# Optimization experiments

Measured on AMD Instinct MI355X. Metric: run time of the kernel, lower is better.

Reference implementation:

```python
import jax, jax.numpy as jnp
import numpy as np

D_MODEL = 256
HEADS = 4
HEAD_DIM = D_MODEL // HEADS  # 64
BN_EPS = 1e-5


def conv1(x, W, b):
    # Conv1d kernel_size=1 == per-position linear: x [B,C,N], W [O,C], b [O]
    return jnp.einsum('oc,bcn->bon', W, x) + b[:, None]


def setup_inputs() -> dict:
    key = jax.random.key(0)
    ks = jax.random.split(key, 12)
    B, N, M = 4, 4096, 4096
    s = 0.02
    return {
        'x': jax.random.normal(ks[0], (B, D_MODEL, N), jnp.float32),
        'source': jax.random.normal(ks[1], (B, D_MODEL, M), jnp.float32),
        'pq_w': jax.random.normal(ks[2], (D_MODEL, D_MODEL), jnp.float32) * s,
        'pq_b': jnp.zeros((D_MODEL,), jnp.float32),
        'pk_w': jax.random.normal(ks[3], (D_MODEL, D_MODEL), jnp.float32) * s,
        'pk_b': jnp.zeros((D_MODEL,), jnp.float32),
        'pv_w': jax.random.normal(ks[4], (D_MODEL, D_MODEL), jnp.float32) * s,
        'pv_b': jnp.zeros((D_MODEL,), jnp.float32),
        'merge_w': jax.random.normal(ks[5], (D_MODEL, D_MODEL), jnp.float32) * s,
        'merge_b': jnp.zeros((D_MODEL,), jnp.float32),
        'mlp1_w': jax.random.normal(ks[6], (2 * D_MODEL, 2 * D_MODEL), jnp.float32) * s,
        'mlp1_b': jax.random.normal(ks[7], (2 * D_MODEL,), jnp.float32) * s,
        'bn_gamma': jnp.ones((2 * D_MODEL,), jnp.float32),
        'bn_beta': jnp.zeros((2 * D_MODEL,), jnp.float32),
        'mlp2_w': jax.random.normal(ks[8], (D_MODEL, 2 * D_MODEL), jnp.float32) * s,
        'mlp2_b': jnp.zeros((D_MODEL,), jnp.float32),  # nn.init.constant_(mlp[-1].bias, 0.0)
    }


def reference(x, source, pq_w, pq_b, pk_w, pk_b, pv_w, pv_b,
              merge_w, merge_b, mlp1_w, mlp1_b, bn_gamma, bn_beta,
              mlp2_w, mlp2_b):
    B = x.shape[0]
    # projections; torch view(B, dim, heads, -1): channels split as (head_dim, heads)
    q = conv1(x, pq_w, pq_b).reshape(B, HEAD_DIM, HEADS, -1)       # [B,d,h,N]
    k = conv1(source, pk_w, pk_b).reshape(B, HEAD_DIM, HEADS, -1)  # [B,d,h,M]
    v = conv1(source, pv_w, pv_b).reshape(B, HEAD_DIM, HEADS, -1)
    scores = jnp.einsum('bdhn,bdhm->bhnm', q, k) / (HEAD_DIM ** 0.5)
    prob = jax.nn.softmax(scores, axis=-1)                          # [B,h,N,M]
    attn_out = jnp.einsum('bhnm,bdhm->bdhn', prob, v).reshape(B, D_MODEL, -1)
    message = conv1(attn_out, merge_w, merge_b)                     # [B,D,N]
    # MLP: conv(512->512) + BatchNorm1d (training-mode batch stats) + ReLU + conv(512->256)
    h = conv1(jnp.concatenate([x, message], axis=1), mlp1_w, mlp1_b)  # [B,2D,N]
    mean = jnp.mean(h, axis=(0, 2), keepdims=True)
    var = jnp.var(h, axis=(0, 2), keepdims=True)  # biased, as torch BN uses for normalization
    h = bn_gamma[:, None] * (h - mean) * jax.lax.rsqrt(var + BN_EPS) + bn_beta[:, None]
    h = jax.nn.relu(h)
    return conv1(h, mlp2_w, mlp2_b)
```

## Files before the change

### kernel.cpp

```cpp
#include <hip/hip_runtime.h>
#include <hip/hip_bf16.h>

#define D_MODEL 256
#define HEADS 4
#define HD 64
#define BATCH 4
#define SEQ 4096
#define NPOS (BATCH*SEQ)
#define SCALE_LOG2 0.18033688011112042f
#define MCHUNKS 2

typedef __attribute__((ext_vector_type(4))) float floatx4;
typedef __attribute__((ext_vector_type(8))) short bf16x8;
typedef __attribute__((ext_vector_type(4))) short bf16x4;
typedef __attribute__((ext_vector_type(4))) unsigned short ushortx4;

__device__ __forceinline__ float bf2f(unsigned short b) {
    return __uint_as_float(((unsigned int)b) << 16);
}
__device__ __forceinline__ unsigned short f2bf(float f) {
    unsigned int u = __float_as_uint(f);
    return (unsigned short)((u + 0x7fffu + ((u >> 16) & 1u)) >> 16);
}
__device__ __forceinline__ bf16x4 pack_bf16x4(float a, float b, float c, float d) {
    __hip_bfloat162 lo = __float22bfloat162_rn(float2{a, b});
    __hip_bfloat162 hi = __float22bfloat162_rn(float2{c, d});
    union { __hip_bfloat162 h2[2]; bf16x4 v; } u;
    u.h2[0] = lo; u.h2[1] = hi;
    return u.v;
}
__device__ __forceinline__ bf16x8 pack_bf16x8(floatx4 a, floatx4 b) {
    union { bf16x4 h[2]; bf16x8 v; } u;
    u.h[0] = pack_bf16x4(a[0], a[1], a[2], a[3]);
    u.h[1] = pack_bf16x4(b[0], b[1], b[2], b[3]);
    return u.v;
}
#define MFMA(a,b,c) __builtin_amdgcn_mfma_f32_16x16x32_bf16((a),(b),(c),0,0,0)
#define EXP2(x) __builtin_amdgcn_exp2f(x)

__global__ __launch_bounds__(256) void prep(
        const float* __restrict__ pq_w, const float* __restrict__ pk_w,
        const float* __restrict__ pv_w, const float* __restrict__ merge_w,
        const float* __restrict__ mlp1_w, const float* __restrict__ mlp2_w,
        const float* __restrict__ x, const float* __restrict__ src,
        unsigned short* __restrict__ wqb, unsigned short* __restrict__ wkb,
        unsigned short* __restrict__ wvb, unsigned short* __restrict__ wmt,
        unsigned short* __restrict__ w1b, unsigned short* __restrict__ w2b,
        unsigned short* __restrict__ xT, unsigned short* __restrict__ srcT)
{
    __shared__ unsigned short lT[64][264];
    const int t = threadIdx.x;
    const int bx = blockIdx.x;
    if (bx < 576) {
        int linear = bx * 1024 + t * 4;
        const float* srcW; unsigned short* dst; int off;
        if (linear < 65536)       { srcW = pq_w;   dst = wqb; off = 0; }
        else if (linear < 131072) { srcW = pk_w;   dst = wkb; off = 65536; }
        else if (linear < 196608) { srcW = pv_w;   dst = wvb; off = 131072; }
        else if (linear < 458752) { srcW = mlp1_w; dst = w1b; off = 196608; }
        else                      { srcW = mlp2_w; dst = w2b; off = 458752; }
        int i = linear - off;
        float4 w = *(const float4*)&srcW[i];
        ushortx4 s = { f2bf(w.x), f2bf(w.y), f2bf(w.z), f2bf(w.w) };
        *(ushortx4*)&dst[i] = s;
        return;
    }
    if (bx < 640) {
        int i = (bx - 576) * 1024 + t * 4;
        int cp = i >> 8, o = i & 255;
        int pc = ((cp & 63) << 2) | (cp >> 6);
        unsigned short s[4];
#pragma unroll
        for (int j = 0; j < 4; ++j)
            s[j] = f2bf(merge_w[(size_t)(o + j) * 256 + pc]);
        *(ushortx4*)&wmt[i] = *(const ushortx4*)s;
        return;
    }
    int z = bx - 640;
    const float* X = (z < 256) ? x : src;
    unsigned short* O = (z < 256) ? xT : srcT;
    int rem = z & 255;
    int b = rem >> 6, n0 = (rem & 63) * 64;
#pragma unroll
    for (int r = 0; r < 16; ++r) {
        int idx = r * 256 + t;
        int ch = idx >> 4, nnq = (idx & 15) * 4;
        float4 v4 = *(const float4*)&X[((size_t)b * 256 + ch) * SEQ + n0 + nnq];
        lT[nnq + 0][ch] = f2bf(v4.x);
        lT[nnq + 1][ch] = f2bf(v4.y);
        lT[nnq + 2][ch] = f2bf(v4.z);
        lT[nnq + 3][ch] = f2bf(v4.w);
    }
    __syncthreads();
#pragma unroll
    for (int r = 0; r < 8; ++r) {
        int idx = r * 256 + t;
        int row = idx >> 5, cg = (idx & 31) * 8;
        *(bf16x8*)&O[((size_t)b * SEQ + n0 + row) * 256 + cg] = *(const bf16x8*)&lT[row][cg];
    }
}

__global__ __launch_bounds__(256) void prep2(
        const float* __restrict__ mlp1_w, const float* __restrict__ mlp1_b,
        const float* __restrict__ merge_b, const unsigned short* __restrict__ wmt,
        unsigned short* __restrict__ w1f, float* __restrict__ b1f)
{
    __shared__ unsigned short lA[64][40];
    __shared__ unsigned short lB[128][40];
    const int t = threadIdx.x;
    if (blockIdx.y == 8) {
        int o2 = blockIdx.x * 256 + t;
        float s = mlp1_b[o2];
        for (int o = 0; o < 256; ++o)
            s += mlp1_w[(size_t)o2 * 512 + 256 + o] * merge_b[o];
        b1f[o2] = s;
        return;
    }
    const int lane = t & 63, wid = t >> 6;
    const int wm = wid >> 1, wn = wid & 1;
    const int lrow = lane & 15, quad = lane >> 4;
    const int o20 = blockIdx.y * 64;
    const int c0  = blockIdx.x * 128;

    floatx4 acc[2][4];
#pragma unroll
    for (int i = 0; i < 2; ++i)
#pragma unroll
        for (int j = 0; j < 4; ++j) acc[i][j] = (floatx4){0.f,0.f,0.f,0.f};

    for (int k0 = 0; k0 < 256; k0 += 32) {
#pragma unroll
        for (int r = 0; r < 2; ++r) {
            int linear = r * 1024 + t * 4;
            int row = linear >> 5, col = linear & 31;
            float4 w = *(const float4*)&mlp1_w[(size_t)(o20 + row) * 512 + 256 + k0 + col];
            ushortx4 s = { f2bf(w.x), f2bf(w.y), f2bf(w.z), f2bf(w.w) };
            *(ushortx4*)&lA[row][col] = s;
        }
#pragma unroll
        for (int r = 0; r < 2; ++r) {
            int linear = r * 256 + t;
            int row = linear >> 2, cg = (linear & 3) * 8;
            *(bf16x8*)&lB[row][cg] = *(const bf16x8*)&wmt[(size_t)(c0 + row) * 256 + k0 + cg];
        }
        __syncthreads();
        bf16x8 aF[2], bF[4];
        const int kq = quad * 8;
#pragma unroll
        for (int mt = 0; mt < 2; ++mt)
            aF[mt] = *(const bf16x8*)&lA[wm*32 + mt*16 + lrow][kq];
#pragma unroll
        for (int nt = 0; nt < 4; ++nt)
            bF[nt] = *(const bf16x8*)&lB[wn*64 + nt*16 + lrow][kq];
#pragma unroll
        for (int mt = 0; mt < 2; ++mt)
#pragma unroll
            for (int nt = 0; nt < 4; ++nt)
                acc[mt][nt] = MFMA(aF[mt], bF[nt], acc[mt][nt]);
        __syncthreads();
    }
#pragma unroll
    for (int nt = 0; nt < 4; ++nt) {
        int cp = c0 + wn*64 + nt*16 + lrow;
#pragma unroll
        for (int mt = 0; mt < 2; ++mt)
#pragma unroll
            for (int j = 0; j < 4; ++j) {
                int o2 = o20 + wm*32 + mt*16 + quad*4 + j;
                w1f[(size_t)o2 * 256 + cp] = f2bf(acc[mt][nt][j]);
            }
    }
}

__global__ __launch_bounds__(256) void proj_qkv_all(
        const unsigned short* __restrict__ Wq, const float* __restrict__ bq,
        const unsigned short* __restrict__ Wk, const float* __restrict__ bk,
        const unsigned short* __restrict__ Wv, const float* __restrict__ bv,
        const unsigned short* __restrict__ xT, const unsigned short* __restrict__ srcT,
        unsigned short* __restrict__ qo, unsigned short* __restrict__ ko,
        unsigned short* __restrict__ vo)
{
    __shared__ unsigned short smem[128 * 80];
    unsigned short (*lA)[40] = (unsigned short (*)[40])smem;
    unsigned short (*lB)[40] = (unsigned short (*)[40])(smem + 128 * 40);
    unsigned short (*stage)[72] = (unsigned short (*)[72])smem;
    const int t = threadIdx.x;
    const int lane = t & 63, wid = t >> 6;
    const int wm = wid >> 1, wn = wid & 1;
    const int lrow = lane & 15, quad = lane >> 4;
    const int mode = blockIdx.x >> 1;
    const int ob = (blockIdx.x & 1) * 128;
    const int n0 = blockIdx.y * 128;
    const int b  = blockIdx.z;
    const unsigned short* W  = (mode == 0) ? Wq : (mode == 1) ? Wk : Wv;
    const float* bias        = (mode == 0) ? bq : (mode == 1) ? bk : bv;
    const unsigned short* XT = (mode == 0) ? xT : srcT;
    unsigned short* out      = (mode == 0) ? qo : (mode == 1) ? ko : vo;

    const int srow[2] = { (0*256 + t) >> 2, (1*256 + t) >> 2 };
    const int scg = (t & 3) * 8;

    floatx4 acc[4][4];
#pragma unroll
    for (int i = 0; i < 4; ++i)
#pragma unroll
        for (int j = 0; j < 4; ++j) acc[i][j] = (floatx4){0.f,0.f,0.f,0.f};

    bf16x8 rW[2], rX[2];
#pragma unroll
    for (int r = 0; r < 2; ++r) {
        rW[r] = *(const bf16x8*)&W[(size_t)(ob + srow[r]) * 256 + scg];
        rX[r] = *(const bf16x8*)&XT[((size_t)b * SEQ + n0 + srow[r]) * 256 + scg];
    }
#pragma unroll
    for (int r = 0; r < 2; ++r) {
        *(bf16x8*)&lA[srow[r]][scg] = rW[r];
        *(bf16x8*)&lB[srow[r]][scg] = rX[r];
    }
    __syncthreads();

    for (int kc = 0; kc < 8; ++kc) {
        const bool pre = (kc + 1 < 8);
        if (pre) {
            const int k1 = (kc + 1) * 32;
#pragma unroll
            for (int r = 0; r < 2; ++r) {
                rW[r] = *(const bf16x8*)&W[(size_t)(ob + srow[r]) * 256 + k1 + scg];
                rX[r] = *(const bf16x8*)&XT[((size_t)b * SEQ + n0 + srow[r]) * 256 + k1 + scg];
            }
        }
        bf16x8 aF[4], bF[4];
        const int kq = quad * 8;
#pragma unroll
        for (int mt = 0; mt < 4; ++mt)
            aF[mt] = *(const bf16x8*)&lA[wm*64 + mt*16 + lrow][kq];
#pragma unroll
        for (int nt = 0; nt < 4; ++nt)
            bF[nt] = *(const bf16x8*)&lB[wn*64 + nt*16 + lrow][kq];
#pragma unroll
        for (int mt = 0; mt < 4; ++mt)
#pragma unroll
            for (int nt = 0; nt < 4; ++nt)
                acc[mt][nt] = MFMA(aF[mt], bF[nt], acc[mt][nt]);
        __syncthreads();
        if (pre) {
#pragma unroll
            for (int r = 0; r < 2; ++r) {
                *(bf16x8*)&lA[srow[r]][scg] = rW[r];
                *(bf16x8*)&lB[srow[r]][scg] = rX[r];
            }
            __syncthreads();
        }
    }
    const float osc = (mode == 0) ? SCALE_LOG2 : 1.0f;
    if (mode == 2) {
#pragma unroll
        for (int mt = 0; mt < 4; ++mt) {
#pragma unroll
            for (int j = 0; j < 4; ++j) {
                int o = ob + wm*64 + mt*16 + quad*4 + j;
                float bvv = bias[o];
                int d = o >> 2, h = o & 3;
#pragma unroll
                for (int nt = 0; nt < 4; ++nt) {
                    int n = n0 + wn*64 + nt*16 + lrow;
                    out[((size_t)(b*HEADS + h) * HD + d) * SEQ + n] = f2bf(acc[mt][nt][j] + bvv);
                }
            }
        }
        return;
    }
    for (int half = 0; half < 2; ++half) {
        __syncthreads();
        if (wm == half) {
#pragma unroll
            for (int mt = 0; mt < 4; ++mt)
#pragma unroll
                for (int j = 0; j < 4; ++j) {
                    int o = ob + half*64 + mt*16 + quad*4 + j;
                    float bvv = bias[o];
                    int col = j*16 + mt*4 + quad;
#pragma unroll
                    for (int nt = 0; nt < 4; ++nt) {
                        int n = wn*64 + nt*16 + lrow;
                        stage[n][col] = f2bf((acc[mt][nt][j] + bvv) * osc);
                    }
                }
        }
        __syncthreads();
#pragma unroll
        for (int i = 0; i < 4; ++i) {
            int c = i * 256 + t;
            int n = c >> 3, h = (c >> 1) & 3, sub = c & 1;
            bf16x8 val = *(const bf16x8*)&stage[n][h*16 + sub*8];
            int d0 = (ob >> 2) + half*16 + sub*8;
            *(bf16x8*)&out[((size_t)(b*HEADS + h) * SEQ + n0 + n) * HD + d0] = val;
        }
    }
}

__global__ __launch_bounds__(256, 4) void flash_attn(
        const unsigned short* __restrict__ q,
        const unsigned short* __restrict__ k,
        const unsigned short* __restrict__ v,
        unsigned short* __restrict__ poO, float* __restrict__ pol)
{
    __shared__ unsigned short smem[2][9216];
    const int t = threadIdx.x, lane = t & 63, wid = t >> 6;
    const int lrow = lane & 15, quad = lane >> 4;
    const int bc = blockIdx.x, qt = blockIdx.y;
    const int bh = bc & 15, chunk = bc >> 4;
    const int hb = (bh & 3) * BATCH + (bh >> 2);
    const int r0 = qt * 128 + wid * 32;

    bf16x8 qf[2][2];
#pragma unroll
    for (int nh = 0; nh < 2; ++nh) {
        const size_t base = ((size_t)bh * SEQ + r0 + nh*16 + lrow) * HD;
        qf[nh][0] = *(const bf16x8*)&q[base + quad * 8];
        qf[nh][1] = *(const bf16x8*)&q[base + 32 + quad * 8];
    }
    bf16x8 ones;
#pragma unroll
    for (int i = 0; i < 8; ++i) ones[i] = (short)0x3F80;
    int mmv[2], cgv[2], krv[2];
#pragma unroll
    for (int r = 0; r < 2; ++r) {
        int linear = r * 256 + t;
        int mm = linear >> 3, cg = (linear & 7) * 8;
        int c2 = mm >> 5, mp = mm & 31;
        mmv[r] = mm; cgv[r] = cg;
        krv[r] = (c2 << 5) + ((mp & 4) << 2) + ((mp >> 3) << 2) + (mp & 3);
    }
    const size_t kbase = ((size_t)bh * SEQ + chunk * (SEQ/MCHUNKS));
    const size_t vbase = (size_t)bh * HD;
    const int moff = chunk * (SEQ/MCHUNKS);
    const int NIT = SEQ / MCHUNKS / 64;

    floatx4 oacc[2][4], oaccL[2];
#pragma unroll
    for (int nh = 0; nh < 2; ++nh) {
        oaccL[nh] = (floatx4){0.f,0.f,0.f,0.f};
#pragma unroll
        for (int i = 0; i < 4; ++i) oacc[nh][i] = (floatx4){0.f,0.f,0.f,0.f};
    }

    {
        bf16x8 pk[2], pv[2];
#pragma unroll
        for (int r = 0; r < 2; ++r) {
            pk[r] = *(const bf16x8*)&k[(kbase + mmv[r]) * HD + cgv[r]];
            pv[r] = *(const bf16x8*)&v[(vbase + mmv[r]) * SEQ + moff + cgv[r]];
        }
#pragma unroll
        for (int r = 0; r < 2; ++r) {
            *(bf16x8*)&smem[0][krv[r]*72 + cgv[r]]        = pk[r];
            *(bf16x8*)&smem[0][4608 + mmv[r]*72 + cgv[r]] = pv[r];
        }
    }
    __syncthreads();

    int p = 0;
#pragma unroll 1
    for (int it = 0; it < NIT; ++it) {
        bf16x8 pk[2], pv[2];
        const bool pre = (it + 1 < NIT);
        if (pre) {
            const int m1 = (it + 1) * 64;
#pragma unroll
            for (int r = 0; r < 2; ++r) {
                pk[r] = *(const bf16x8*)&k[(kbase + m1 + mmv[r]) * HD + cgv[r]];
                pv[r] = *(const bf16x8*)&v[(vbase + mmv[r]) * SEQ + moff + m1 + cgv[r]];
            }
        }
        const unsigned short* lK = smem[p];
        const unsigned short* lV = smem[p] + 4608;

        bf16x8 pf8[2][2];
#pragma unroll
        for (int c2 = 0; c2 < 2; ++c2) {
            floatx4 sa[2][2];
#pragma unroll
            for (int AB = 0; AB < 2; ++AB) {
                sa[AB][0] = (floatx4){0.f,0.f,0.f,0.f};
                sa[AB][1] = (floatx4){0.f,0.f,0.f,0.f};
#pragma unroll
                for (int kc = 0; kc < 2; ++kc) {
                    bf16x8 kf = *(const bf16x8*)&lK[(c2*32 + AB*16 + lrow)*72 + kc*32 + quad*8];
                    sa[AB][0] = MFMA(kf, qf[0][kc], sa[AB][0]);
                    sa[AB][1] = MFMA(kf, qf[1][kc], sa[AB][1]);
                }
            }
#pragma unroll
            for (int nh = 0; nh < 2; ++nh) {
                floatx4 ea, eb;
#pragma unroll
                for (int i = 0; i < 4; ++i) { ea[i] = EXP2(sa[0][nh][i]); eb[i] = EXP2(sa[1][nh][i]); }
                pf8[c2][nh] = pack_bf16x8(ea, eb);
            }
        }
#pragma unroll
        for (int c2 = 0; c2 < 2; ++c2) {
            oaccL[0] = MFMA(ones, pf8[c2][0], oaccL[0]);
            oaccL[1] = MFMA(ones, pf8[c2][1], oaccL[1]);
#pragma unroll
            for (int dt = 0; dt < 4; ++dt) {
                bf16x8 vf = *(const bf16x8*)&lV[(dt*16 + lrow)*72 + c2*32 + quad*8];
                oacc[0][dt] = MFMA(vf, pf8[c2][0], oacc[0][dt]);
                oacc[1][dt] = MFMA(vf, pf8[c2][1], oacc[1][dt]);
            }
        }
        if (pre) {
#pragma unroll
            for (int r = 0; r < 2; ++r) {
                *(bf16x8*)&smem[p^1][krv[r]*72 + cgv[r]]        = pk[r];
                *(bf16x8*)&smem[p^1][4608 + mmv[r]*72 + cgv[r]] = pv[r];
            }
        }
        __syncthreads();
        p ^= 1;
    }
    const size_t prow = (size_t)(chunk*16 + hb) * SEQ + qt * 128;
    if (lane < 16) {
        pol[prow + wid*32 + lrow]      = oaccL[0][0];
        pol[prow + wid*32 + 16 + lrow] = oaccL[1][0];
    }
    unsigned short* stB = (unsigned short*)&smem[0][0];
#pragma unroll
    for (int nh = 0; nh < 2; ++nh)
#pragma unroll
        for (int dt = 0; dt < 4; ++dt) {
            bf16x4 pv4 = pack_bf16x4(oacc[nh][dt][0], oacc[nh][dt][1],
                                     oacc[nh][dt][2], oacc[nh][dt][3]);
            *(bf16x4*)&stB[(wid*32 + nh*16 + lrow)*72 + dt*16 + quad*4] = pv4;
        }
    __syncthreads();
#pragma unroll
    for (int i = 0; i < 4; ++i) {
        int c = i * 256 + t;
        int row = c >> 3, sub = c & 7;
        *(bf16x8*)&poO[(prow + row) * HD + sub*8] = *(const bf16x8*)&stB[row*72 + sub*8];
    }
}

__global__ __launch_bounds__(256) void gemm_mlp1(
        const unsigned short* __restrict__ xT, const unsigned short* __restrict__ poO,
        const float* __restrict__ pol,
        const unsigned short* __restrict__ w1b, const unsigned short* __restrict__ w1f,
        const float* __restrict__ b1f, unsigned short* __restrict__ h1,
        float* __restrict__ sums, float* __restrict__ sumsq)
{
    __shared__ unsigned short lA[2][64][40];
    __shared__ unsigned short lB[2][128][40];
    __shared__ float sInv[256];
    const int t = threadIdx.x;
    const int lane = t & 63, wid = t >> 6;
    const int wm = wid >> 1, wn = wid & 1;
    const int lrow = lane & 15, quad = lane >> 4;
    const int o0 = blockIdx.x * 128;
    const int p0 = blockIdx.y * 64;
    const int b = p0 >> 12, n0 = p0 & (SEQ - 1);
    const size_t CH = (size_t)16 * SEQ * HD;

    {
        int h = t >> 6, nn = t & 63;
        int hb = h * BATCH + b;
        float l0 = pol[(size_t)hb * SEQ + n0 + nn];
        float l1 = pol[(size_t)(16 + hb) * SEQ + n0 + nn];
        sInv[t] = 1.0f / (l0 + l1);
    }
    __syncthreads();

    const int arow = t >> 2, acg = (t & 3) * 8;
    const int brow[2] = { (0*256 + t) >> 2, (1*256 + t) >> 2 };

    floatx4 acc[2][4];
#pragma unroll
    for (int i = 0; i < 2; ++i)
#pragma unroll
        for (int j = 0; j < 4; ++j) acc[i][j] = (floatx4){0.f,0.f,0.f,0.f};

    bf16x8 rA, rB[2];
    auto load_tile = [&](int k0) {
        if (k0 < 256) {
            rA = *(const bf16x8*)&xT[(size_t)(p0 + arow) * 256 + k0 + acg];
#pragma unroll
            for (int r = 0; r < 2; ++r)
                rB[r] = *(const bf16x8*)&w1b[(size_t)(o0 + brow[r]) * 512 + k0 + acg];
        } else {
            const int kk2 = k0 - 256;
            const int h = kk2 >> 6, d0 = kk2 & 63, hb = h * BATCH + b;
            const unsigned short* bse = &poO[((size_t)hb * SEQ + n0 + arow) * HD + d0 + acg];
            bf16x8 a0 = *(const bf16x8*)bse;
            bf16x8 a1 = *(const bf16x8*)(bse + CH);
            float inv = sInv[h*64 + arow];
            unsigned short res[8];
#pragma unroll
            for (int i = 0; i < 8; ++i)
                res[i] = f2bf((bf2f((unsigned short)a0[i]) + bf2f((unsigned short)a1[i])) * inv);
            rA = *(const bf16x8*)res;
#pragma unroll
            for (int r = 0; r < 2; ++r)
                rB[r] = *(const bf16x8*)&w1f[(size_t)(o0 + brow[r]) * 256 + kk2 + acg];
        }
    };

    load_tile(0);
    *(bf16x8*)&lA[0][arow][acg] = rA;
#pragma unroll
    for (int r = 0; r < 2; ++r) *(bf16x8*)&lB[0][brow[r]][acg] = rB[r];
    __syncthreads();

    int p = 0;
    for (int kc = 0; kc < 16; ++kc) {
        const bool pre = (kc + 1 < 16);
        if (pre) load_tile((kc + 1) * 32);
        bf16x8 aF[2], bF[4];
        const int kq = quad * 8;
#pragma unroll
        for (int mt = 0; mt < 2; ++mt)
            aF[mt] = *(const bf16x8*)&lA[p][wm*32 + mt*16 + lrow][kq];
#pragma unroll
        for (int nt = 0; nt < 4; ++nt)
            bF[nt] = *(const bf16x8*)&lB[p][wn*64 + nt*16 + lrow][kq];
#pragma unroll
        for (int mt = 0; mt < 2; ++mt)
#pragma unroll
            for (int nt = 0; nt < 4; ++nt)
                acc[mt][nt] = MFMA(aF[mt], bF[nt], acc[mt][nt]);
        if (pre) {
            *(bf16x8*)&lA[p^1][arow][acg] = rA;
#pragma unroll
            for (int r = 0; r < 2; ++r) *(bf16x8*)&lB[p^1][brow[r]][acg] = rB[r];
        }
        __syncthreads();
        p ^= 1;
    }
#pragma unroll
    for (int nt = 0; nt < 4; ++nt) {
        int o = o0 + wn*64 + nt*16 + lrow;
        float bvv = b1f[o];
        float s = 0.f, qs = 0.f;
#pragma unroll
        for (int mt = 0; mt < 2; ++mt)
#pragma unroll
            for (int j = 0; j < 4; ++j) {
                int pos = p0 + wm*32 + mt*16 + quad*4 + j;
                float val = acc[mt][nt][j] + bvv;
                h1[(size_t)pos * 512 + o] = f2bf(val);
                s += val; qs += val * val;
            }
        s  += __shfl_xor(s, 16);  s  += __shfl_xor(s, 32);
        qs += __shfl_xor(qs, 16); qs += __shfl_xor(qs, 32);
        if (lane < 16) {
            atomicAdd(&sums[o], s);
            atomicAdd(&sumsq[o], qs);
        }
    }
}

__global__ __launch_bounds__(256) void gemm_mlp2(
        const unsigned short* __restrict__ W2, const unsigned short* __restrict__ h1,
        const float* __restrict__ bias,
        const float* __restrict__ sums, const float* __restrict__ sumsq,
        const float* __restrict__ gamma, const float* __restrict__ beta,
        float* __restrict__ out)
{
    __shared__ unsigned short lA[2][128][40];
    __shared__ unsigned short lB[2][64][40];
    __shared__ float sSc[512], sSh[512];
    const int t = threadIdx.x;
    const int lane = t & 63, wid = t >> 6;
    const int wm = wid >> 1, wn = wid & 1;
    const int lrow = lane & 15, quad = lane >> 4;
    const int o0 = blockIdx.x * 128;
    const int p0 = blockIdx.y * 64;

#pragma unroll
    for (int cc = 0; cc < 2; ++cc) {
        int c = cc * 256 + t;
        float mean = sums[c] * (1.0f / NPOS);
        float var  = sumsq[c] * (1.0f / NPOS) - mean * mean;
        float sc = gamma[c] * rsqrtf(var + 1e-5f);
        sSc[c] = sc;
        sSh[c] = beta[c] - mean * sc;
    }
    __syncthreads();

    const int arow[2] = { (0*256 + t) >> 2, (1*256 + t) >> 2 };
    const int acg = (t & 3) * 8;
    const int brow = t >> 2;

    floatx4 acc[4][2];
#pragma unroll
    for (int i = 0; i < 4; ++i)
#pragma unroll
        for (int j = 0; j < 2; ++j) acc[i][j] = (floatx4){0.f,0.f,0.f,0.f};

    bf16x8 rW[2], rH;
    auto load_tile = [&](int k0) {
#pragma unroll
        for (int r = 0; r < 2; ++r)
            rW[r] = *(const bf16x8*)&W2[(size_t)(o0 + arow[r]) * 512 + k0 + acg];
        bf16x8 hv = *(const bf16x8*)&h1[(size_t)(p0 + brow) * 512 + k0 + acg];
        unsigned short res[8];
#pragma unroll
        for (int i = 0; i < 8; ++i) {
            int c = k0 + acg + i;
            float f = bf2f((unsigned short)hv[i]);
            f = fmaxf(f * sSc[c] + sSh[c], 0.f);
            res[i] = f2bf(f);
        }
        rH = *(const bf16x8*)res;
    };

    load_tile(0);
#pragma unroll
    for (int r = 0; r < 2; ++r) *(bf16x8*)&lA[0][arow[r]][acg] = rW[r];
    *(bf16x8*)&lB[0][brow][acg] = rH;
    __syncthreads();

    int p = 0;
    for (int kc = 0; kc < 16; ++kc) {
        const bool pre = (kc + 1 < 16);
        if (pre) load_tile((kc + 1) * 32);
        bf16x8 aF[4], bF[2];
        const int kq = quad * 8;
#pragma unroll
        for (int mt = 0; mt < 4; ++mt)
            aF[mt] = *(const bf16x8*)&lA[p][wm*64 + mt*16 + lrow][kq];
#pragma unroll
        for (int nt = 0; nt < 2; ++nt)
            bF[nt] = *(const bf16x8*)&lB[p][wn*32 + nt*16 + lrow][kq];
#pragma unroll
        for (int mt = 0; mt < 4; ++mt)
#pragma unroll
            for (int nt = 0; nt < 2; ++nt)
                acc[mt][nt] = MFMA(aF[mt], bF[nt], acc[mt][nt]);
        if (pre) {
#pragma unroll
            for (int r = 0; r < 2; ++r) *(bf16x8*)&lA[p^1][arow[r]][acg] = rW[r];
            *(bf16x8*)&lB[p^1][brow][acg] = rH;
        }
        __syncthreads();
        p ^= 1;
    }
#pragma unroll
    for (int mt = 0; mt < 4; ++mt)
#pragma unroll
        for (int j = 0; j < 4; ++j) {
            int o = o0 + wm*64 + mt*16 + quad*4 + j;
            float bvv = bias[o];
#pragma unroll
            for (int nt = 0; nt < 2; ++nt) {
                int pos = p0 + wn*32 + nt*16 + lrow;
                int b = pos >> 12, n = pos & (SEQ - 1);
                out[((size_t)b * D_MODEL + o) * SEQ + n] = acc[mt][nt][j] + bvv;
            }
        }
}

extern "C" void kernel_launch(void* const* d_in, const int* in_sizes, int n_in,
                              void* d_out, int out_size, void* d_ws, size_t ws_size,
                              hipStream_t stream)
{
    (void)in_sizes; (void)n_in; (void)out_size; (void)ws_size;
    const float* x        = (const float*)d_in[0];
    const float* source   = (const float*)d_in[1];
    const float* pq_w     = (const float*)d_in[2];
    const float* pq_b     = (const float*)d_in[3];
    const float* pk_w     = (const float*)d_in[4];
    const float* pk_b     = (const float*)d_in[5];
    const float* pv_w     = (const float*)d_in[6];
    const float* pv_b     = (const float*)d_in[7];
    const float* merge_w  = (const float*)d_in[8];
    const float* merge_b  = (const float*)d_in[9];
    const float* mlp1_w   = (const float*)d_in[10];
    const float* mlp1_b   = (const float*)d_in[11];
    const float* bn_gamma = (const float*)d_in[12];
    const float* bn_beta  = (const float*)d_in[13];
    const float* mlp2_w   = (const float*)d_in[14];
    const float* mlp2_b   = (const float*)d_in[15];
    float* out = (float*)d_out;

    char* ws = (char*)d_ws;
    const size_t MB = 1ull << 20;
    unsigned short* xT   = (unsigned short*)(ws);
    unsigned short* srcT = (unsigned short*)(ws + 8*MB);
    unsigned short* q    = (unsigned short*)(ws + 16*MB);
    unsigned short* kk   = (unsigned short*)(ws + 24*MB);
    unsigned short* v    = (unsigned short*)(ws + 32*MB);
    unsigned short* poO  = (unsigned short*)(ws + 40*MB);
    unsigned short* h1   = (unsigned short*)(ws + 57*MB);
    float* pol = (float*)(ws + 73*MB);
    unsigned short* wqb = (unsigned short*)(ws + 74*MB);
    unsigned short* wkb = wqb + 65536;
    unsigned short* wvb = wkb + 65536;
    unsigned short* wmt = wvb + 65536;
    unsigned short* w1b = wmt + 65536;
    unsigned short* w2b = w1b + 262144;
    unsigned short* w1f = w2b + 131072;
    float* b1f = (float*)(w1f + 131072);
    float* bn_sum = b1f + 512;
    float* bn_sumsq = bn_sum + 512;

    hipMemsetAsync(bn_sum, 0, 1024 * sizeof(float), stream);

    prep<<<dim3(1152), 256, 0, stream>>>(
        pq_w, pk_w, pv_w, merge_w, mlp1_w, mlp2_w, x, source,
        wqb, wkb, wvb, wmt, w1b, w2b, xT, srcT);
    prep2<<<dim3(2, 9), 256, 0, stream>>>(mlp1_w, mlp1_b, merge_b, wmt, w1f, b1f);
    proj_qkv_all<<<dim3(6, SEQ/128, BATCH), 256, 0, stream>>>(
        wqb, pq_b, wkb, pk_b, wvb, pv_b, xT, srcT, q, kk, v);
    flash_attn<<<dim3(16*MCHUNKS, SEQ/128), 256, 0, stream>>>(q, kk, v, poO, pol);
    gemm_mlp1<<<dim3(4, NPOS/64), 256, 0, stream>>>(
        xT, poO, pol, w1b, w1f, b1f, h1, bn_sum, bn_sumsq);
    gemm_mlp2<<<dim3(2, NPOS/64), 256, 0, stream>>>(
        w2b, h1, mlp2_b, bn_sum, bn_sumsq, bn_gamma, bn_beta, out);
}
```

Before: 272.2 us.

## Split attention KV into four chunks, XOR-swizzle LDS, and raise MFMA priority

Doubles the number of KV split chunks in flash attention so more blocks run concurrently, and updates the MLP1 GEMM to sum four partial outputs and normalizers. Replaces the padded 72-stride LDS layout with a 64-stride XOR-swizzled layout, shrinking shared memory and allowing an occupancy hint of 5 blocks. Wraps the MFMA sections in s_setprio to favor matrix issue. It costs more partial-output traffic and extra reduction work in the GEMM, and it reuses the q workspace region for h1.

Result: slower. 638.4 us (+134.6%).

```diff
diff --git a/kernel.cpp b/kernel.cpp
--- a/kernel.cpp
+++ b/kernel.cpp
@@ -8,7 +8,7 @@
 #define SEQ 4096
 #define NPOS (BATCH*SEQ)
 #define SCALE_LOG2 0.18033688011112042f
-#define MCHUNKS 2
+#define MCHUNKS 4
 
 typedef __attribute__((ext_vector_type(4))) float floatx4;
 typedef __attribute__((ext_vector_type(8))) short bf16x8;
@@ -299,15 +299,16 @@
     }
 }
 
-__global__ __launch_bounds__(256, 4) void flash_attn(
+__global__ __launch_bounds__(256, 5) void flash_attn(
         const unsigned short* __restrict__ q,
         const unsigned short* __restrict__ k,
         const unsigned short* __restrict__ v,
         unsigned short* __restrict__ poO, float* __restrict__ pol)
 {
-    __shared__ unsigned short smem[2][9216];
+    __shared__ unsigned short smem[2][8192];
     const int t = threadIdx.x, lane = t & 63, wid = t >> 6;
     const int lrow = lane & 15, quad = lane >> 4;
+    const int xq = lane & 7;
     const int bc = blockIdx.x, qt = blockIdx.y;
     const int bh = bc & 15, chunk = bc >> 4;
     const int hb = (bh & 3) * BATCH + (bh >> 2);
@@ -323,14 +324,16 @@
     bf16x8 ones;
 #pragma unroll
     for (int i = 0; i < 8; ++i) ones[i] = (short)0x3F80;
-    int mmv[2], cgv[2], krv[2];
+    int mmv[2], cgv[2], kwo[2], vwo[2];
 #pragma unroll
     for (int r = 0; r < 2; ++r) {
         int linear = r * 256 + t;
         int mm = linear >> 3, cg = (linear & 7) * 8;
         int c2 = mm >> 5, mp = mm & 31;
+        int krv = (c2 << 5) + ((mp & 4) << 2) + ((mp >> 3) << 2) + (mp & 3);
         mmv[r] = mm; cgv[r] = cg;
-        krv[r] = (c2 << 5) + ((mp & 4) << 2) + ((mp >> 3) << 2) + (mp & 3);
+        kwo[r] = krv * 64 + (((cg >> 3) ^ (krv & 7)) << 3);
+        vwo[r] = 4096 + mm * 64 + (((cg >> 3) ^ (mm & 7)) << 3);
     }
     const size_t kbase = ((size_t)bh * SEQ + chunk * (SEQ/MCHUNKS));
     const size_t vbase = (size_t)bh * HD;
@@ -354,8 +357,8 @@
         }
 #pragma unroll
         for (int r = 0; r < 2; ++r) {
-            *(bf16x8*)&smem[0][krv[r]*72 + cgv[r]]        = pk[r];
-            *(bf16x8*)&smem[0][4608 + mmv[r]*72 + cgv[r]] = pv[r];
+            *(bf16x8*)&smem[0][kwo[r]] = pk[r];
+            *(bf16x8*)&smem[0][vwo[r]] = pv[r];
         }
     }
     __syncthreads();
@@ -373,8 +376,7 @@
                 pv[r] = *(const bf16x8*)&v[(vbase + mmv[r]) * SEQ + moff + m1 + cgv[r]];
             }
         }
-        const unsigned short* lK = smem[p];
-        const unsigned short* lV = smem[p] + 4608;
+        const unsigned short* lS = smem[p];
 
         bf16x8 pf8[2][2];
 #pragma unroll
@@ -384,13 +386,19 @@
             for (int AB = 0; AB < 2; ++AB) {
                 sa[AB][0] = (floatx4){0.f,0.f,0.f,0.f};
                 sa[AB][1] = (floatx4){0.f,0.f,0.f,0.f};
+            }
+            __builtin_amdgcn_s_setprio(1);
+#pragma unroll
+            for (int AB = 0; AB < 2; ++AB) {
 #pragma unroll
                 for (int kc = 0; kc < 2; ++kc) {
-                    bf16x8 kf = *(const bf16x8*)&lK[(c2*32 + AB*16 + lrow)*72 + kc*32 + quad*8];
+                    bf16x8 kf = *(const bf16x8*)&lS[(c2*32 + AB*16 + lrow)*64
+                                                    + (((kc*4 + quad) ^ xq) << 3)];
                     sa[AB][0] = MFMA(kf, qf[0][kc], sa[AB][0]);
                     sa[AB][1] = MFMA(kf, qf[1][kc], sa[AB][1]);
                 }
             }
+            __builtin_amdgcn_s_setprio(0);
 #pragma unroll
             for (int nh = 0; nh < 2; ++nh) {
                 floatx4 ea, eb;
@@ -399,22 +407,25 @@
                 pf8[c2][nh] = pack_bf16x8(ea, eb);
             }
         }
+        __builtin_amdgcn_s_setprio(1);
 #pragma unroll
         for (int c2 = 0; c2 < 2; ++c2) {
             oaccL[0] = MFMA(ones, pf8[c2][0], oaccL[0]);
             oaccL[1] = MFMA(ones, pf8[c2][1], oaccL[1]);
 #pragma unroll
             for (int dt = 0; dt < 4; ++dt) {
-                bf16x8 vf = *(const bf16x8*)&lV[(dt*16 + lrow)*72 + c2*32 + quad*8];
+                bf16x8 vf = *(const bf16x8*)&lS[4096 + (dt*16 + lrow)*64
+                                                + (((c2*4 + quad) ^ xq) << 3)];
                 oacc[0][dt] = MFMA(vf, pf8[c2][0], oacc[0][dt]);
                 oacc[1][dt] = MFMA(vf, pf8[c2][1], oacc[1][dt]);
             }
         }
+        __builtin_amdgcn_s_setprio(0);
         if (pre) {
 #pragma unroll
             for (int r = 0; r < 2; ++r) {
-                *(bf16x8*)&smem[p^1][krv[r]*72 + cgv[r]]        = pk[r];
-                *(bf16x8*)&smem[p^1][4608 + mmv[r]*72 + cgv[r]] = pv[r];
+                *(bf16x8*)&smem[p^1][kwo[r]] = pk[r];
+                *(bf16x8*)&smem[p^1][vwo[r]] = pv[r];
             }
         }
         __syncthreads();
@@ -432,14 +443,17 @@
         for (int dt = 0; dt < 4; ++dt) {
             bf16x4 pv4 = pack_bf16x4(oacc[nh][dt][0], oacc[nh][dt][1],
                                      oacc[nh][dt][2], oacc[nh][dt][3]);
-            *(bf16x4*)&stB[(wid*32 + nh*16 + lrow)*72 + dt*16 + quad*4] = pv4;
+            int row = wid*32 + nh*16 + lrow;
+            int blk = dt*2 + (quad >> 1);
+            *(bf16x4*)&stB[row*64 + ((blk ^ xq) << 3) + (quad & 1)*4] = pv4;
         }
     __syncthreads();
 #pragma unroll
     for (int i = 0; i < 4; ++i) {
         int c = i * 256 + t;
         int row = c >> 3, sub = c & 7;
-        *(bf16x8*)&poO[(prow + row) * HD + sub*8] = *(const bf16x8*)&stB[row*72 + sub*8];
+        *(bf16x8*)&poO[(prow + row) * HD + sub*8] =
+            *(const bf16x8*)&stB[row*64 + ((sub ^ (row & 7)) << 3)];
     }
 }
 
@@ -465,9 +479,11 @@
     {
         int h = t >> 6, nn = t & 63;
         int hb = h * BATCH + b;
-        float l0 = pol[(size_t)hb * SEQ + n0 + nn];
-        float l1 = pol[(size_t)(16 + hb) * SEQ + n0 + nn];
-        sInv[t] = 1.0f / (l0 + l1);
+        float l = 0.f;
+#pragma unroll
+        for (int c = 0; c < MCHUNKS; ++c)
+            l += pol[((size_t)(c*16 + hb)) * SEQ + n0 + nn];
+        sInv[t] = 1.0f / l;
     }
     __syncthreads();
 
@@ -491,13 +507,21 @@
             const int kk2 = k0 - 256;
             const int h = kk2 >> 6, d0 = kk2 & 63, hb = h * BATCH + b;
             const unsigned short* bse = &poO[((size_t)hb * SEQ + n0 + arow) * HD + d0 + acg];
-            bf16x8 a0 = *(const bf16x8*)bse;
-            bf16x8 a1 = *(const bf16x8*)(bse + CH);
             float inv = sInv[h*64 + arow];
+            float fs[8];
+#pragma unroll
+            for (int i = 0; i < 8; ++i) fs[i] = 0.f;
+#pragma unroll
+            for (int c = 0; c < MCHUNKS; ++c) {
+                bf16x8 a = *(const bf16x8*)(bse + (size_t)c * CH);
+#pragma unroll
+                for (int i = 0; i < 8; ++i)
+                    fs[i] += bf2f((unsigned short)a[i]);
+            }
             unsigned short res[8];
 #pragma unroll
             for (int i = 0; i < 8; ++i)
-                res[i] = f2bf((bf2f((unsigned short)a0[i]) + bf2f((unsigned short)a1[i])) * inv);
+                res[i] = f2bf(fs[i] * inv);
             rA = *(const bf16x8*)res;
 #pragma unroll
             for (int r = 0; r < 2; ++r)
@@ -691,9 +715,9 @@
     unsigned short* kk   = (unsigned short*)(ws + 24*MB);
     unsigned short* v    = (unsigned short*)(ws + 32*MB);
     unsigned short* poO  = (unsigned short*)(ws + 40*MB);
-    unsigned short* h1   = (unsigned short*)(ws + 57*MB);
-    float* pol = (float*)(ws + 73*MB);
-    unsigned short* wqb = (unsigned short*)(ws + 74*MB);
+    unsigned short* h1   = (unsigned short*)(ws + 16*MB);
+    float* pol = (float*)(ws + 72*MB);
+    unsigned short* wqb = (unsigned short*)(ws + 73*MB);
     unsigned short* wkb = wqb + 65536;
     unsigned short* wvb = wkb + 65536;
     unsigned short* wmt = wvb + 65536;
```
